# Kernel tuning notes

Hardware: AMD Instinct MI355X
Metric: run time of the kernel (lower is better)

The kernel has to match this reference:

```python
import jax, jax.numpy as jnp
import numpy as np

NDIM = 7  # window side; N = 49
NUM_HEADS = 12

def _rel_pos_index(ndim=NDIM):
    coords = np.stack(np.meshgrid(np.arange(ndim), np.arange(ndim), indexing='ij'))  # [2,7,7]
    cf = coords.reshape(2, -1)                      # [2,49]
    rel = cf[:, :, None] - cf[:, None, :]           # [2,49,49]
    rel = rel.transpose(1, 2, 0).copy()             # [49,49,2]
    rel[:, :, 0] += ndim - 1
    rel[:, :, 1] += ndim - 1
    rel[:, :, 0] *= 2 * ndim - 1
    return jnp.asarray(rel.sum(-1), dtype=jnp.int32)  # [49,49]

def setup_inputs() -> dict:
    key = jax.random.key(0)
    ks = jax.random.split(key, 6)
    B, N, C = 1024, NDIM * NDIM, 768
    x = jax.random.normal(ks[0], (B, N, C), dtype=jnp.float32)
    prev = jax.random.normal(ks[1], (B, NUM_HEADS, N, N), dtype=jnp.float32)
    # weights stored as [in, out] so forward is x @ W (matches torch Linear math)
    qkv_w = jax.random.normal(ks[2], (C, 3 * C), dtype=jnp.float32) * 0.02
    proj_w = jax.random.normal(ks[3], (C, C), dtype=jnp.float32) * 0.02
    proj_b = jax.random.normal(ks[4], (C,), dtype=jnp.float32) * 0.02
    bias_table = jax.random.normal(ks[5], ((2 * NDIM - 1) ** 2, NUM_HEADS), dtype=jnp.float32) * 0.02
    rel_idx = _rel_pos_index()
    return {"x": x, "prev": prev, "qkv_w": qkv_w, "proj_w": proj_w,
            "proj_b": proj_b, "bias_table": bias_table, "rel_idx": rel_idx}

def reference(x, prev, qkv_w, proj_w, proj_b, bias_table, rel_idx):
    B, N, C = x.shape
    H = NUM_HEADS
    hd = C // H
    scale = hd ** -0.5
    qkv = (x @ qkv_w).reshape(B, N, 3, H, hd)
    q = qkv[:, :, 0].transpose(0, 2, 1, 3)  # [B,H,N,hd]
    k = qkv[:, :, 1].transpose(0, 2, 1, 3)
    v = qkv[:, :, 2].transpose(0, 2, 1, 3)
    attn_score = jnp.einsum('bhnd,bhmd->bhnm', q, k) * scale  # [B,H,N,N]
    bias = bias_table[rel_idx.reshape(-1)].reshape(N, N, H).transpose(2, 0, 1)  # [H,N,N]
    attn_score = attn_score + bias[None]
    attn_score = attn_score + prev          # res_score=True path
    prev_out = attn_score
    attn = jax.nn.softmax(attn_score, axis=-1)
    out = jnp.einsum('bhnm,bhmd->bhnd', attn, v).transpose(0, 2, 1, 3).reshape(B, N, C)
    out = out @ proj_w + proj_b
    return (out, prev_out)
```

## Files before the change

kernel.cpp:

```cpp
#include <hip/hip_runtime.h>

typedef unsigned short u16;
typedef unsigned int u32;
typedef float f32x4 __attribute__((ext_vector_type(4)));
typedef __bf16 bf16x8 __attribute__((ext_vector_type(8)));

#define DEV static __device__ __forceinline__

DEV u16 f2bf(float f) {
  u32 u = __builtin_bit_cast(u32, f);
  u += 0x7fffu + ((u >> 16) & 1u);
  return (u16)(u >> 16);
}

DEV void gload_lds16(const void* g, void* l) {
  __builtin_amdgcn_global_load_lds(
      (const __attribute__((address_space(1))) u32*)g,
      (__attribute__((address_space(3))) u32*)l, 16, 0, 0);
}


__global__ __launch_bounds__(256) void cvt_bf16(const float* __restrict__ in,
                                                u16* __restrict__ out, int n4) {
  int i = blockIdx.x * 256 + threadIdx.x;
  const int stride = gridDim.x * 256;
  for (; i < n4; i += stride) {
    const float4 v = ((const float4*)in)[i];
    ushort4 o;
    o.x = f2bf(v.x); o.y = f2bf(v.y); o.z = f2bf(v.z); o.w = f2bf(v.w);
    ((ushort4*)out)[i] = o;
  }
}

__global__ __launch_bounds__(256) void cvtT_bf16(const float* __restrict__ in,
                                                 u16* __restrict__ out, int K, int N) {
  int i = blockIdx.x * 256 + threadIdx.x;
  if (i >= N * K) return;
  int n = i / K, k = i - n * K;
  out[i] = f2bf(in[(long)k * N + n]);
}

__global__ __launch_bounds__(256) void bias_pre(const float* __restrict__ bias_table,
                                                const int* __restrict__ rel_idx,
                                                float* __restrict__ biasM) {
  int i = blockIdx.x * 256 + threadIdx.x;
  if (i >= 12 * 2401) return;
  int h = i / 2401, p = i - h * 2401;
  biasM[i] = bias_table[rel_idx[p] * 12 + h];
}

template <bool OUT_BF16>
__global__ __launch_bounds__(512, 2) void gemm256(
    const u16* __restrict__ A, const u16* __restrict__ BT,
    void* __restrict__ C, const float* __restrict__ bias,
    int M, int N, int K, int nbn) {
  __shared__ alignas(16) char lds[131072];
  const int t = threadIdx.x;
  const int w = t >> 6, l = t & 63, lr = l & 15, lhi = l >> 4;
  const int wr = w >> 2, wc = w & 3;

  const int nwg = gridDim.x;
  const int q = nwg >> 3, r = nwg & 7;
  const int xcd = blockIdx.x & 7, lid = blockIdx.x >> 3;
  const int swz = (xcd < r ? xcd * (q + 1) : r * (q + 1) + (xcd - r) * q) + lid;
  const int bm = swz / nbn, bn = swz % nbn;

  const int T = K >> 5;
  const long Kb = (long)K * 2;

  const int unswz = (l & 7) ^ (l >> 3);
  const int arow = 2 * (l >> 3) + (unswz >> 2);
  const int acolb = (unswz & 3) << 4;
  const char* gA0 = (const char*)A + (long)(bm * 256 + w * 32 + arow) * Kb + acolb;
  const char* gA1 = gA0 + 16 * Kb;
  const char* gB0 = (const char*)BT + (long)(bn * 256 + w * 32 + arow) * Kb + acolb;
  const char* gB1 = gB0 + 16 * Kb;
  const int ldA0 = w * 2048, ldA1 = w * 2048 + 1024;
  const int ldB0 = 16384 + w * 2048, ldB1 = 16384 + w * 2048 + 1024;

#define STAGE(tt)                               \
  {                                             \
    const int bb = ((tt) & 3) * 32768;          \
    const long ko = (long)(tt) * 64;            \
    gload_lds16(gA0 + ko, lds + bb + ldA0);     \
    gload_lds16(gA1 + ko, lds + bb + ldA1);     \
    gload_lds16(gB0 + ko, lds + bb + ldB0);     \
    gload_lds16(gB1 + ko, lds + bb + ldB1);     \
  }
#define VMCNT8 asm volatile("s_waitcnt vmcnt(8)" ::: "memory")
#define BAR                                  \
  asm volatile("" ::: "memory");             \
  __builtin_amdgcn_s_barrier();              \
  asm volatile("" ::: "memory")

  const int rblk = ((((lr & 1) << 2) | lhi) ^ (lr >> 1));
  const int aoff0 = (wr * 64 + (lr >> 1)) * 128 + rblk * 16;
  const int boff0 = 16384 + (wc * 32 + (lr >> 1)) * 128 + rblk * 16;

  f32x4 acc[8][4];
#pragma unroll
  for (int m = 0; m < 8; ++m)
#pragma unroll
    for (int n = 0; n < 4; ++n) acc[m][n] = (f32x4){0.f, 0.f, 0.f, 0.f};
  bf16x8 afr[8], bfr[4];

  STAGE(0); STAGE(1); STAGE(2);
  VMCNT8;
  BAR;
#pragma unroll
  for (int n = 0; n < 4; ++n) bfr[n] = *(const bf16x8*)(lds + boff0 + n * 1024);
#pragma unroll
  for (int m = 0; m < 4; ++m) afr[m] = *(const bf16x8*)(lds + aoff0 + m * 1024);

  for (int kt = 0; kt < T; ++kt) {
    if (kt + 3 < T) STAGE(kt + 3);
    {
      const int bb = (kt & 3) * 32768;
#pragma unroll
      for (int m = 4; m < 8; ++m)
        afr[m] = *(const bf16x8*)(lds + bb + aoff0 + m * 1024);
    }
    __builtin_amdgcn_s_setprio(1);
#pragma unroll
    for (int m = 0; m < 4; ++m)
#pragma unroll
      for (int n = 0; n < 4; ++n)
        acc[m][n] = __builtin_amdgcn_mfma_f32_16x16x32_bf16(afr[m], bfr[n], acc[m][n], 0, 0, 0);
    __builtin_amdgcn_s_setprio(0);
    __builtin_amdgcn_s_setprio(1);
#pragma unroll
    for (int m = 4; m < 8; ++m)
#pragma unroll
      for (int n = 0; n < 4; ++n)
        acc[m][n] = __builtin_amdgcn_mfma_f32_16x16x32_bf16(afr[m], bfr[n], acc[m][n], 0, 0, 0);
    __builtin_amdgcn_s_setprio(0);
    VMCNT8;
    BAR;
    if (kt + 1 < T) {
      const int bb = ((kt + 1) & 3) * 32768;
#pragma unroll
      for (int n = 0; n < 4; ++n)
        bfr[n] = *(const bf16x8*)(lds + bb + boff0 + n * 1024);
#pragma unroll
      for (int m = 0; m < 4; ++m)
        afr[m] = *(const bf16x8*)(lds + bb + aoff0 + m * 1024);
    }
  }
#undef STAGE
#undef VMCNT8
#undef BAR

  const int row0 = bm * 256 + wr * 128 + 4 * lhi;
  const int col0 = bn * 256 + wc * 64 + lr;
  if (OUT_BF16) {
    u16* Cc = (u16*)C;
#pragma unroll
    for (int m = 0; m < 8; ++m)
#pragma unroll
      for (int rr = 0; rr < 4; ++rr) {
        const long row = row0 + m * 16 + rr;
#pragma unroll
        for (int n = 0; n < 4; ++n)
          Cc[row * N + col0 + n * 16] = f2bf(acc[m][n][rr]);
      }
  } else {
    float* Cf = (float*)C;
    float bv[4];
#pragma unroll
    for (int n = 0; n < 4; ++n) bv[n] = bias[col0 + n * 16];
#pragma unroll
    for (int m = 0; m < 8; ++m)
#pragma unroll
      for (int rr = 0; rr < 4; ++rr) {
        const long row = row0 + m * 16 + rr;
#pragma unroll
        for (int n = 0; n < 4; ++n)
          Cf[row * N + col0 + n * 16] = acc[m][n][rr] + bv[n];
      }
  }
}

__global__ __launch_bounds__(256) void attn_kernel(
    const u16* __restrict__ qkv,
    const float* __restrict__ prev,
    const float* __restrict__ biasM,
    float* __restrict__ prev_out,
    u16* __restrict__ attn_out) {
  __shared__ u16 Qs[64][72];
  __shared__ u16 Ks[64][72];
  __shared__ u16 VTs[64][72];
  __shared__ float SB[2432];

  const int bh = blockIdx.x;
  const int b = bh / 12, h = bh % 12;
  const int t = threadIdx.x, w = t >> 6, l = t & 63, lr = l & 15, lhi = l >> 4;

  const u16* base = qkv + (long)(b * 49) * 2304 + h * 64;
  for (int idx = t; idx < 49 * 16; idx += 256) {
    const int n = idx >> 4, c4 = (idx & 15) << 2;
    const u16* rp = base + (long)n * 2304;
    ushort4 qv = *(const ushort4*)(rp + c4);
    ushort4 kv = *(const ushort4*)(rp + 768 + c4);
    ushort4 vv = *(const ushort4*)(rp + 1536 + c4);
    *(ushort4*)&Qs[n][c4] = qv;
    *(ushort4*)&Ks[n][c4] = kv;
    VTs[c4 + 0][n] = vv.x;
    VTs[c4 + 1][n] = vv.y;
    VTs[c4 + 2][n] = vv.z;
    VTs[c4 + 3][n] = vv.w;
  }
  for (int idx = t; idx < 1024; idx += 256) {
    const int j = idx & 15;
    if (j) VTs[idx >> 4][48 + j] = 0;
  }
  {
    const float* pv = prev + (long)bh * 2401;
    const float* bm = biasM + h * 2401;
    for (int i = t; i < 2401; i += 256) SB[i] = pv[i] + bm[i];
  }
  __syncthreads();

  bf16x8 af0 = *(const bf16x8*)&Qs[16 * w + lr][lhi * 8];
  bf16x8 af1 = *(const bf16x8*)&Qs[16 * w + lr][32 + lhi * 8];
  f32x4 sacc[4];
#pragma unroll
  for (int tc = 0; tc < 4; ++tc) {
    sacc[tc] = (f32x4){0.f, 0.f, 0.f, 0.f};
    bf16x8 b0 = *(const bf16x8*)&Ks[16 * tc + lr][lhi * 8];
    bf16x8 b1 = *(const bf16x8*)&Ks[16 * tc + lr][32 + lhi * 8];
    sacc[tc] = __builtin_amdgcn_mfma_f32_16x16x32_bf16(af0, b0, sacc[tc], 0, 0, 0);
    sacc[tc] = __builtin_amdgcn_mfma_f32_16x16x32_bf16(af1, b1, sacc[tc], 0, 0, 0);
  }

  u16 (*Ps)[72] = Qs;
  const int nrow0 = 16 * w + 4 * lhi;
  float rs[4];
#pragma unroll
  for (int r = 0; r < 4; ++r) {
    const int row = nrow0 + r;
    const bool rv = row < 49;
    float sv[4];
#pragma unroll
    for (int tc = 0; tc < 4; ++tc) {
      const int col = 16 * tc + lr;
      const bool valid = rv && (col < 49);
      const int sidx = (row < 49 ? row : 48) * 49 + (col < 49 ? col : 48);
      const float pb = SB[sidx];
      const float s = sacc[tc][r] * 0.125f + pb;
      if (valid) SB[sidx] = s;
      sv[tc] = valid ? s : -INFINITY;
    }
    float mx = fmaxf(fmaxf(sv[0], sv[1]), fmaxf(sv[2], sv[3]));
#pragma unroll
    for (int off = 8; off; off >>= 1) mx = fmaxf(mx, __shfl_xor(mx, off, 16));
    float e[4], sum = 0.f;
#pragma unroll
    for (int tc = 0; tc < 4; ++tc) {
      e[tc] = __expf(sv[tc] - mx);
      sum += e[tc];
    }
#pragma unroll
    for (int off = 8; off; off >>= 1) sum += __shfl_xor(sum, off, 16);
    rs[r] = 1.0f / sum;
#pragma unroll
    for (int tc = 0; tc < 4; ++tc)
      Ps[row][16 * tc + lr] = rv ? f2bf(e[tc]) : (u16)0;
  }
  __syncthreads();

  bf16x8 pf0 = *(const bf16x8*)&Ps[16 * w + lr][lhi * 8];
  bf16x8 pf1 = *(const bf16x8*)&Ps[16 * w + lr][32 + lhi * 8];
  f32x4 oacc[4];
#pragma unroll
  for (int dc = 0; dc < 4; ++dc) {
    oacc[dc] = (f32x4){0.f, 0.f, 0.f, 0.f};
    bf16x8 v0 = *(const bf16x8*)&VTs[16 * dc + lr][lhi * 8];
    bf16x8 v1 = *(const bf16x8*)&VTs[16 * dc + lr][32 + lhi * 8];
    oacc[dc] = __builtin_amdgcn_mfma_f32_16x16x32_bf16(pf0, v0, oacc[dc], 0, 0, 0);
    oacc[dc] = __builtin_amdgcn_mfma_f32_16x16x32_bf16(pf1, v1, oacc[dc], 0, 0, 0);
  }
  u16* ob = attn_out + (long)(b * 49) * 768 + h * 64;
#pragma unroll
  for (int r = 0; r < 4; ++r) {
    const int row = nrow0 + r;
    if (row < 49) {
#pragma unroll
      for (int dc = 0; dc < 4; ++dc)
        ob[(long)row * 768 + 16 * dc + lr] = f2bf(oacc[dc][r] * rs[r]);
    }
  }

  {
    float* pout = prev_out + (long)bh * 2401;
    for (int i = t; i < 2401; i += 256) pout[i] = SB[i];
  }
}

extern "C" void kernel_launch(void* const* d_in, const int* in_sizes, int n_in,
                              void* d_out, int out_size, void* d_ws, size_t ws_size,
                              hipStream_t stream) {
  const float* x = (const float*)d_in[0];
  const float* prev = (const float*)d_in[1];
  const float* qkv_w = (const float*)d_in[2];
  const float* proj_w = (const float*)d_in[3];
  const float* proj_b = (const float*)d_in[4];
  const float* bias_table = (const float*)d_in[5];
  const int* rel_idx = (const int*)d_in[6];

  const int B = in_sizes[0] / (49 * 768);
  const int M = B * 49;

  float* out0 = (float*)d_out;
  float* out1 = out0 + (size_t)M * 768;

  char* ws = (char*)d_ws;
  u16* xbf = (u16*)ws;
  u16* qkvbf = (u16*)(ws + (size_t)M * 768 * 2);
  u16* qkvwT = (u16*)(ws + (size_t)M * 768 * 2 + (size_t)M * 2304 * 2);
  u16* projwT = qkvwT + 2304 * 768;
  float* biasM = (float*)(projwT + 768 * 768);

  bias_pre<<<(12 * 2401 + 255) / 256, 256, 0, stream>>>(bias_table, rel_idx, biasM);
  cvt_bf16<<<2048, 256, 0, stream>>>(x, xbf, M * 768 / 4);
  cvtT_bf16<<<(2304 * 768 + 255) / 256, 256, 0, stream>>>(qkv_w, qkvwT, 768, 2304);
  cvtT_bf16<<<(768 * 768 + 255) / 256, 256, 0, stream>>>(proj_w, projwT, 768, 768);

  gemm256<true><<<(M / 256) * (2304 / 256), 512, 0, stream>>>(
      xbf, qkvwT, qkvbf, nullptr, M, 2304, 768, 2304 / 256);

  attn_kernel<<<B * 12, 256, 0, stream>>>(qkvbf, prev, biasM, out1, xbf);

  gemm256<false><<<(M / 256) * (768 / 256), 512, 0, stream>>>(
      xbf, projwT, out0, proj_b, M, 768, 768, 768 / 256);
}
```

Before: 536.1 us.

## Software-pipeline LDS fragment loads between MFMA clusters with ping-pong registers

Unrolls the GEMM K-loop by two and switches to ping-pong register fragment sets (X/Y). The next tile's B and A fragments are now read from LDS between the two MFMA clusters of the current tile, rather than after the barrier. The global-load wait becomes vmcnt(4), which keeps two stages landed ahead so those early reads stay safe. This is meant to hide LDS read latency behind MFMA work, at the cost of more registers, less prefetch slack, and an assumption that the K tile count is even.

```diff
diff --git a/kernel.cpp b/kernel.cpp
--- a/kernel.cpp
+++ b/kernel.cpp
@@ -87,7 +87,6 @@
     gload_lds16(gB0 + ko, lds + bb + ldB0);     \
     gload_lds16(gB1 + ko, lds + bb + ldB1);     \
   }
-#define VMCNT8 asm volatile("s_waitcnt vmcnt(8)" ::: "memory")
 #define BAR                                  \
   asm volatile("" ::: "memory");             \
   __builtin_amdgcn_s_barrier();              \
@@ -102,53 +101,63 @@
   for (int m = 0; m < 8; ++m)
 #pragma unroll
     for (int n = 0; n < 4; ++n) acc[m][n] = (f32x4){0.f, 0.f, 0.f, 0.f};
-  bf16x8 afr[8], bfr[4];
+  bf16x8 afrX[4], bfrX[4], afrY[4], bfrY[4];
+
+#define CLUSTER1(S)                                                        \
+  __builtin_amdgcn_s_setprio(1);                                           \
+  _Pragma("unroll") for (int m = 0; m < 4; ++m)                            \
+      _Pragma("unroll") for (int n = 0; n < 4; ++n)                        \
+          acc[m][n] = __builtin_amdgcn_mfma_f32_16x16x32_bf16(             \
+              afr##S[m], bfr##S[n], acc[m][n], 0, 0, 0);                   \
+  __builtin_amdgcn_s_setprio(0)
+#define CLUSTER2(S)                                                        \
+  __builtin_amdgcn_s_setprio(1);                                           \
+  _Pragma("unroll") for (int m = 0; m < 4; ++m)                            \
+      _Pragma("unroll") for (int n = 0; n < 4; ++n)                        \
+          acc[m + 4][n] = __builtin_amdgcn_mfma_f32_16x16x32_bf16(         \
+              afr2[m], bfr##S[n], acc[m + 4][n], 0, 0, 0);                 \
+  __builtin_amdgcn_s_setprio(0)
+
+#define BODY(kt, S, R)                                                     \
+  {                                                                        \
+    if ((kt) + 3 < T) STAGE((kt) + 3);                                     \
+    const int bbc = ((kt) & 3) * 32768;                                    \
+    const int nx = ((kt) + 1 < T) ? (kt) + 1 : (kt);                       \
+    const int bbn = (nx & 3) * 32768;                                      \
+    bf16x8 afr2[4];                                                        \
+    _Pragma("unroll") for (int m = 0; m < 4; ++m)                          \
+        afr2[m] = *(const bf16x8*)(lds + bbc + aoff0 + (m + 4) * 1024);    \
+    CLUSTER1(S);                                                           \
+    _Pragma("unroll") for (int n = 0; n < 4; ++n)                          \
+        bfr##R[n] = *(const bf16x8*)(lds + bbn + boff0 + n * 1024);        \
+    CLUSTER2(S);                                                           \
+    _Pragma("unroll") for (int m = 0; m < 4; ++m)                          \
+        afr##R[m] = *(const bf16x8*)(lds + bbn + aoff0 + m * 1024);        \
+    if ((kt) + 3 < T) {                                                    \
+      asm volatile("s_waitcnt vmcnt(4)" ::: "memory");                     \
+    } else {                                                               \
+      asm volatile("s_waitcnt vmcnt(0)" ::: "memory");                     \
+    }                                                                      \
+    BAR;                                                                   \
+  }
 
   STAGE(0); STAGE(1); STAGE(2);
-  VMCNT8;
+  asm volatile("s_waitcnt vmcnt(4)" ::: "memory");
   BAR;
 #pragma unroll
-  for (int n = 0; n < 4; ++n) bfr[n] = *(const bf16x8*)(lds + boff0 + n * 1024);
-#pragma unroll
-  for (int m = 0; m < 4; ++m) afr[m] = *(const bf16x8*)(lds + aoff0 + m * 1024);
-
-  for (int kt = 0; kt < T; ++kt) {
-    if (kt + 3 < T) STAGE(kt + 3);
-    {
-      const int bb = (kt & 3) * 32768;
-#pragma unroll
-      for (int m = 4; m < 8; ++m)
-        afr[m] = *(const bf16x8*)(lds + bb + aoff0 + m * 1024);
-    }
-    __builtin_amdgcn_s_setprio(1);
-#pragma unroll
-    for (int m = 0; m < 4; ++m)
-#pragma unroll
-      for (int n = 0; n < 4; ++n)
-        acc[m][n] = __builtin_amdgcn_mfma_f32_16x16x32_bf16(afr[m], bfr[n], acc[m][n], 0, 0, 0);
-    __builtin_amdgcn_s_setprio(0);
-    __builtin_amdgcn_s_setprio(1);
-#pragma unroll
-    for (int m = 4; m < 8; ++m)
-#pragma unroll
-      for (int n = 0; n < 4; ++n)
-        acc[m][n] = __builtin_amdgcn_mfma_f32_16x16x32_bf16(afr[m], bfr[n], acc[m][n], 0, 0, 0);
-    __builtin_amdgcn_s_setprio(0);
-    VMCNT8;
-    BAR;
-    if (kt + 1 < T) {
-      const int bb = ((kt + 1) & 3) * 32768;
-#pragma unroll
-      for (int n = 0; n < 4; ++n)
-        bfr[n] = *(const bf16x8*)(lds + bb + boff0 + n * 1024);
-#pragma unroll
-      for (int m = 0; m < 4; ++m)
-        afr[m] = *(const bf16x8*)(lds + bb + aoff0 + m * 1024);
-    }
+  for (int n = 0; n < 4; ++n) bfrX[n] = *(const bf16x8*)(lds + boff0 + n * 1024);
+#pragma unroll
+  for (int m = 0; m < 4; ++m) afrX[m] = *(const bf16x8*)(lds + aoff0 + m * 1024);
+
+  for (int i = 0; i < T / 2; ++i) {
+    BODY(2 * i, X, Y);
+    BODY(2 * i + 1, Y, X);
   }
 #undef STAGE
-#undef VMCNT8
 #undef BAR
+#undef CLUSTER1
+#undef CLUSTER2
+#undef BODY
 
   const int row0 = bm * 256 + wr * 128 + 4 * lhi;
   const int col0 = bn * 256 + wc * 64 + lr;
```

Result: no change. 527.0 us (-1.7%).

## Restructure GEMM mainloop to double-buffered 64-wide K tiles with compile-time K

Applied to the files above, without the earlier changes.

The bf16 GEMM mainloop changes from a 4-stage ring of K=32 tiles to a 2-stage double buffer of K=64 tiles, with a new LDS swizzle and fragment layout. Each tile now runs two MFMAs per accumulator, and the next stage's global-to-LDS loads are issued after a mid-iteration barrier so they overlap with the last rows of MFMAs. K is hardcoded to 768, with T=12 and constant offsets, which lets the compiler fold address arithmetic. In exchange the prefetch depth drops from three tiles ahead to one, and the kernel only works for K=768.

```diff
diff --git a/kernel.cpp b/kernel.cpp
--- a/kernel.cpp
+++ b/kernel.cpp
@@ -53,7 +53,9 @@
 __global__ __launch_bounds__(512, 2) void gemm256(
     const u16* __restrict__ A, const u16* __restrict__ BT,
     void* __restrict__ C, const float* __restrict__ bias,
-    int M, int N, int K, int nbn) {
+    int M, int N, int nbn) {
+  constexpr int T = 12;
+  constexpr long Kb = 768 * 2;
   __shared__ alignas(16) char lds[131072];
   const int t = threadIdx.x;
   const int w = t >> 6, l = t & 63, lr = l & 15, lhi = l >> 4;
@@ -65,89 +67,88 @@
   const int swz = (xcd < r ? xcd * (q + 1) : r * (q + 1) + (xcd - r) * q) + lid;
   const int bm = swz / nbn, bn = swz % nbn;
 
-  const int T = K >> 5;
-  const long Kb = (long)K * 2;
-
-  const int unswz = (l & 7) ^ (l >> 3);
-  const int arow = 2 * (l >> 3) + (unswz >> 2);
-  const int acolb = (unswz & 3) << 4;
-  const char* gA0 = (const char*)A + (long)(bm * 256 + w * 32 + arow) * Kb + acolb;
-  const char* gA1 = gA0 + 16 * Kb;
-  const char* gB0 = (const char*)BT + (long)(bn * 256 + w * 32 + arow) * Kb + acolb;
-  const char* gB1 = gB0 + 16 * Kb;
-  const int ldA0 = w * 2048, ldA1 = w * 2048 + 1024;
-  const int ldB0 = 16384 + w * 2048, ldB1 = 16384 + w * 2048 + 1024;
-
-#define STAGE(tt)                               \
-  {                                             \
-    const int bb = ((tt) & 3) * 32768;          \
-    const long ko = (long)(tt) * 64;            \
-    gload_lds16(gA0 + ko, lds + bb + ldA0);     \
-    gload_lds16(gA1 + ko, lds + bb + ldA1);     \
-    gload_lds16(gB0 + ko, lds + bb + ldB0);     \
-    gload_lds16(gB1 + ko, lds + bb + ldB1);     \
-  }
-#define VMCNT8 asm volatile("s_waitcnt vmcnt(8)" ::: "memory")
+  const int srow = w * 16 + (l >> 3);
+  const int sb = (l & 7) ^ ((l >> 3) & 7);
+  const char* gAs = (const char*)A + (long)(bm * 256 + srow) * Kb + sb * 16;
+  const char* gBs = (const char*)BT + (long)(bn * 256 + srow) * Kb + sb * 16;
+  const int ldw = w * 2048;
+
+#define STG(tt)                                                        \
+  {                                                                    \
+    const int bb = ((tt) & 1) * 65536;                                 \
+    const long ko = (long)(tt) * 128;                                  \
+    gload_lds16(gAs + ko, lds + bb + ldw);                             \
+    gload_lds16(gAs + 12288 + ko, lds + bb + ldw + 1024);              \
+    gload_lds16(gAs + 196608 + ko, lds + bb + 16384 + ldw);            \
+    gload_lds16(gAs + 208896 + ko, lds + bb + 16384 + ldw + 1024);     \
+    gload_lds16(gBs + ko, lds + bb + 32768 + ldw);                     \
+    gload_lds16(gBs + 12288 + ko, lds + bb + 32768 + ldw + 1024);      \
+    gload_lds16(gBs + 196608 + ko, lds + bb + 49152 + ldw);            \
+    gload_lds16(gBs + 208896 + ko, lds + bb + 49152 + ldw + 1024);     \
+  }
 #define BAR                                  \
   asm volatile("" ::: "memory");             \
   __builtin_amdgcn_s_barrier();              \
   asm volatile("" ::: "memory")
 
-  const int rblk = ((((lr & 1) << 2) | lhi) ^ (lr >> 1));
-  const int aoff0 = (wr * 64 + (lr >> 1)) * 128 + rblk * 16;
-  const int boff0 = 16384 + (wc * 32 + (lr >> 1)) * 128 + rblk * 16;
+  const int aoffL = (wr * 128 + lr) * 128 + ((lhi ^ (lr & 7)) << 4);
+  const int boffL = 32768 + (wc * 64 + lr) * 128 + ((lhi ^ (lr & 7)) << 4);
 
   f32x4 acc[8][4];
 #pragma unroll
   for (int m = 0; m < 8; ++m)
 #pragma unroll
     for (int n = 0; n < 4; ++n) acc[m][n] = (f32x4){0.f, 0.f, 0.f, 0.f};
-  bf16x8 afr[8], bfr[4];
-
-  STAGE(0); STAGE(1); STAGE(2);
-  VMCNT8;
+
+  STG(0); STG(1);
+  asm volatile("s_waitcnt vmcnt(8)" ::: "memory");
   BAR;
-#pragma unroll
-  for (int n = 0; n < 4; ++n) bfr[n] = *(const bf16x8*)(lds + boff0 + n * 1024);
-#pragma unroll
-  for (int m = 0; m < 4; ++m) afr[m] = *(const bf16x8*)(lds + aoff0 + m * 1024);
 
   for (int kt = 0; kt < T; ++kt) {
-    if (kt + 3 < T) STAGE(kt + 3);
-    {
-      const int bb = (kt & 3) * 32768;
-#pragma unroll
-      for (int m = 4; m < 8; ++m)
-        afr[m] = *(const bf16x8*)(lds + bb + aoff0 + m * 1024);
-    }
+    const int bb = (kt & 1) * 65536;
+    bf16x8 bfr[4][2];
+#pragma unroll
+    for (int nt = 0; nt < 4; ++nt) {
+      bfr[nt][0] = *(const bf16x8*)(lds + (bb + boffL + nt * 2048));
+      bfr[nt][1] = *(const bf16x8*)(lds + ((bb + boffL + nt * 2048) ^ 64));
+    }
+#pragma unroll
+    for (int mt = 0; mt < 6; ++mt) {
+      bf16x8 a0 = *(const bf16x8*)(lds + (bb + aoffL + mt * 2048));
+      bf16x8 a1 = *(const bf16x8*)(lds + ((bb + aoffL + mt * 2048) ^ 64));
+      __builtin_amdgcn_s_setprio(1);
+#pragma unroll
+      for (int nt = 0; nt < 4; ++nt) {
+        acc[mt][nt] = __builtin_amdgcn_mfma_f32_16x16x32_bf16(a0, bfr[nt][0], acc[mt][nt], 0, 0, 0);
+        acc[mt][nt] = __builtin_amdgcn_mfma_f32_16x16x32_bf16(a1, bfr[nt][1], acc[mt][nt], 0, 0, 0);
+      }
+      __builtin_amdgcn_s_setprio(0);
+    }
+    bf16x8 a60 = *(const bf16x8*)(lds + (bb + aoffL + 6 * 2048));
+    bf16x8 a61 = *(const bf16x8*)(lds + ((bb + aoffL + 6 * 2048) ^ 64));
+    bf16x8 a70 = *(const bf16x8*)(lds + (bb + aoffL + 7 * 2048));
+    bf16x8 a71 = *(const bf16x8*)(lds + ((bb + aoffL + 7 * 2048) ^ 64));
+    asm volatile("s_waitcnt lgkmcnt(0)" ::: "memory");
+    __builtin_amdgcn_sched_barrier(0);
+    BAR;
+    if (kt + 2 < T) STG(kt + 2);
     __builtin_amdgcn_s_setprio(1);
 #pragma unroll
-    for (int m = 0; m < 4; ++m)
-#pragma unroll
-      for (int n = 0; n < 4; ++n)
-        acc[m][n] = __builtin_amdgcn_mfma_f32_16x16x32_bf16(afr[m], bfr[n], acc[m][n], 0, 0, 0);
+    for (int nt = 0; nt < 4; ++nt) {
+      acc[6][nt] = __builtin_amdgcn_mfma_f32_16x16x32_bf16(a60, bfr[nt][0], acc[6][nt], 0, 0, 0);
+      acc[6][nt] = __builtin_amdgcn_mfma_f32_16x16x32_bf16(a61, bfr[nt][1], acc[6][nt], 0, 0, 0);
+      acc[7][nt] = __builtin_amdgcn_mfma_f32_16x16x32_bf16(a70, bfr[nt][0], acc[7][nt], 0, 0, 0);
+      acc[7][nt] = __builtin_amdgcn_mfma_f32_16x16x32_bf16(a71, bfr[nt][1], acc[7][nt], 0, 0, 0);
+    }
     __builtin_amdgcn_s_setprio(0);
-    __builtin_amdgcn_s_setprio(1);
-#pragma unroll
-    for (int m = 4; m < 8; ++m)
-#pragma unroll
-      for (int n = 0; n < 4; ++n)
-        acc[m][n] = __builtin_amdgcn_mfma_f32_16x16x32_bf16(afr[m], bfr[n], acc[m][n], 0, 0, 0);
-    __builtin_amdgcn_s_setprio(0);
-    VMCNT8;
+    if (kt + 2 < T) {
+      asm volatile("s_waitcnt vmcnt(8)" ::: "memory");
+    } else {
+      asm volatile("s_waitcnt vmcnt(0)" ::: "memory");
+    }
     BAR;
-    if (kt + 1 < T) {
-      const int bb = ((kt + 1) & 3) * 32768;
-#pragma unroll
-      for (int n = 0; n < 4; ++n)
-        bfr[n] = *(const bf16x8*)(lds + bb + boff0 + n * 1024);
-#pragma unroll
-      for (int m = 0; m < 4; ++m)
-        afr[m] = *(const bf16x8*)(lds + bb + aoff0 + m * 1024);
-    }
-  }
-#undef STAGE
-#undef VMCNT8
+  }
+#undef STG
 #undef BAR
 
   const int row0 = bm * 256 + wr * 128 + 4 * lhi;
@@ -326,10 +327,10 @@
   cvtT_bf16<<<(768 * 768 + 255) / 256, 256, 0, stream>>>(proj_w, projwT, 768, 768);
 
   gemm256<true><<<(M / 256) * (2304 / 256), 512, 0, stream>>>(
-      xbf, qkvwT, qkvbf, nullptr, M, 2304, 768, 2304 / 256);
+      xbf, qkvwT, qkvbf, nullptr, M, 2304, 2304 / 256);
 
   attn_kernel<<<B * 12, 256, 0, stream>>>(qkvbf, prev, biasM, out1, xbf);
 
   gemm256<false><<<(M / 256) * (768 / 256), 512, 0, stream>>>(
-      xbf, projwT, out0, proj_b, M, 768, 768, 768 / 256);
-}
+      xbf, projwT, out0, proj_b, M, 768, 768 / 256);
+}
```

Result: no change. 542.5 us (+1.2%).

## Restructure GEMM main loop into two barrier-synchronized phases with split A/B staging

Applied to the files above, without the earlier changes.

Reorganizes the bf16 GEMM inner loop into two half-phases per K-tile. Each phase reads its fragments from LDS, issues half of the next stage's global-to-LDS loads (A, then B), and synchronizes with barriers and lgkmcnt(0) waits before its MFMA block, in a ping-pong style schedule. This replaces the previous prefetch-across-iterations fragment loading and aims to interleave memory issue with MFMA work across waves more evenly. It adds two extra barriers per iteration and drops cross-iteration register prefetch of fragments, which could expose LDS latency.

```diff
diff --git a/kernel.cpp b/kernel.cpp
--- a/kernel.cpp
+++ b/kernel.cpp
@@ -78,20 +78,27 @@
   const int ldA0 = w * 2048, ldA1 = w * 2048 + 1024;
   const int ldB0 = 16384 + w * 2048, ldB1 = 16384 + w * 2048 + 1024;
 
-#define STAGE(tt)                               \
-  {                                             \
-    const int bb = ((tt) & 3) * 32768;          \
-    const long ko = (long)(tt) * 64;            \
-    gload_lds16(gA0 + ko, lds + bb + ldA0);     \
-    gload_lds16(gA1 + ko, lds + bb + ldA1);     \
-    gload_lds16(gB0 + ko, lds + bb + ldB0);     \
-    gload_lds16(gB1 + ko, lds + bb + ldB1);     \
-  }
-#define VMCNT8 asm volatile("s_waitcnt vmcnt(8)" ::: "memory")
+#define STG_A(tt)                                            \
+  {                                                          \
+    const int bb = ((tt) & 3) * 32768;                       \
+    const long ko = (long)(tt) * 64;                         \
+    gload_lds16(gA0 + ko, lds + bb + ldA0);                  \
+    gload_lds16(gA1 + ko, lds + bb + ldA1);                  \
+  }
+#define STG_B(tt)                                            \
+  {                                                          \
+    const int bb = ((tt) & 3) * 32768;                       \
+    const long ko = (long)(tt) * 64;                         \
+    gload_lds16(gB0 + ko, lds + bb + ldB0);                  \
+    gload_lds16(gB1 + ko, lds + bb + ldB1);                  \
+  }
 #define BAR                                  \
   asm volatile("" ::: "memory");             \
   __builtin_amdgcn_s_barrier();              \
   asm volatile("" ::: "memory")
+#define LGKM0                                              \
+  asm volatile("s_waitcnt lgkmcnt(0)" ::: "memory");       \
+  __builtin_amdgcn_sched_barrier(0)
 
   const int rblk = ((((lr & 1) << 2) | lhi) ^ (lr >> 1));
   const int aoff0 = (wr * 64 + (lr >> 1)) * 128 + rblk * 16;
@@ -102,24 +109,24 @@
   for (int m = 0; m < 8; ++m)
 #pragma unroll
     for (int n = 0; n < 4; ++n) acc[m][n] = (f32x4){0.f, 0.f, 0.f, 0.f};
-  bf16x8 afr[8], bfr[4];
-
-  STAGE(0); STAGE(1); STAGE(2);
-  VMCNT8;
+
+  STG_A(0); STG_B(0); STG_A(1); STG_B(1); STG_A(2); STG_B(2);
+  asm volatile("s_waitcnt vmcnt(8)" ::: "memory");
   BAR;
-#pragma unroll
-  for (int n = 0; n < 4; ++n) bfr[n] = *(const bf16x8*)(lds + boff0 + n * 1024);
-#pragma unroll
-  for (int m = 0; m < 4; ++m) afr[m] = *(const bf16x8*)(lds + aoff0 + m * 1024);
 
   for (int kt = 0; kt < T; ++kt) {
-    if (kt + 3 < T) STAGE(kt + 3);
-    {
-      const int bb = (kt & 3) * 32768;
-#pragma unroll
-      for (int m = 4; m < 8; ++m)
-        afr[m] = *(const bf16x8*)(lds + bb + aoff0 + m * 1024);
-    }
+    const int bb = (kt & 3) * 32768;
+    const bool stg = (kt + 3) < T;
+    bf16x8 bfr[4], afr[4];
+#pragma unroll
+    for (int n = 0; n < 4; ++n)
+      bfr[n] = *(const bf16x8*)(lds + bb + boff0 + n * 1024);
+#pragma unroll
+    for (int m = 0; m < 4; ++m)
+      afr[m] = *(const bf16x8*)(lds + bb + aoff0 + m * 1024);
+    if (stg) STG_A(kt + 3);
+    BAR;
+    LGKM0;
     __builtin_amdgcn_s_setprio(1);
 #pragma unroll
     for (int m = 0; m < 4; ++m)
@@ -127,28 +134,32 @@
       for (int n = 0; n < 4; ++n)
         acc[m][n] = __builtin_amdgcn_mfma_f32_16x16x32_bf16(afr[m], bfr[n], acc[m][n], 0, 0, 0);
     __builtin_amdgcn_s_setprio(0);
+    BAR;
+    bf16x8 afr2[4];
+#pragma unroll
+    for (int m = 0; m < 4; ++m)
+      afr2[m] = *(const bf16x8*)(lds + bb + aoff0 + (m + 4) * 1024);
+    if (stg) STG_B(kt + 3);
+    BAR;
+    LGKM0;
     __builtin_amdgcn_s_setprio(1);
 #pragma unroll
-    for (int m = 4; m < 8; ++m)
+    for (int m = 0; m < 4; ++m)
 #pragma unroll
       for (int n = 0; n < 4; ++n)
-        acc[m][n] = __builtin_amdgcn_mfma_f32_16x16x32_bf16(afr[m], bfr[n], acc[m][n], 0, 0, 0);
+        acc[m + 4][n] = __builtin_amdgcn_mfma_f32_16x16x32_bf16(afr2[m], bfr[n], acc[m + 4][n], 0, 0, 0);
     __builtin_amdgcn_s_setprio(0);
-    VMCNT8;
+    if (stg) {
+      asm volatile("s_waitcnt vmcnt(8)" ::: "memory");
+    } else {
+      asm volatile("s_waitcnt vmcnt(0)" ::: "memory");
+    }
     BAR;
-    if (kt + 1 < T) {
-      const int bb = ((kt + 1) & 3) * 32768;
-#pragma unroll
-      for (int n = 0; n < 4; ++n)
-        bfr[n] = *(const bf16x8*)(lds + bb + boff0 + n * 1024);
-#pragma unroll
-      for (int m = 0; m < 4; ++m)
-        afr[m] = *(const bf16x8*)(lds + bb + aoff0 + m * 1024);
-    }
-  }
-#undef STAGE
-#undef VMCNT8
+  }
+#undef STG_A
+#undef STG_B
 #undef BAR
+#undef LGKM0
 
   const int row0 = bm * 256 + wr * 128 + 4 * lhi;
   const int col0 = bn * 256 + wc * 64 + lr;
```

Measured after the change: 542.3 us. About the same (+1.1%).
